# Kernel tuning notes

Measured on AMD Instinct MI355X. Metric: run time of the kernel, lower is better.

The kernel has to match this reference:

```python
import jax, jax.numpy as jnp
import numpy as np
from jax import lax

B, T, N, D = 64, 2048, 64, 128


def setup_inputs() -> dict:
    key = jax.random.key(0)
    k0, k1, k2, k3, k4 = jax.random.split(key, 5)
    return {
        "X": jax.random.normal(k0, (B, T, D), dtype=jnp.float32),
        "transition_matrix": jax.random.uniform(k1, (N, N), dtype=jnp.float32) / N,
        "state_priors": jax.random.uniform(k2, (N,), dtype=jnp.float32) / N,
        "means": jax.random.normal(k3, (N, D), dtype=jnp.float32),
        "log_vars": jax.random.normal(k4, (N, D), dtype=jnp.float32) * 0.1,
    }


def _emission_logprobs(X, means, log_vars):
    # Diagonal-Gaussian log density per state, vectorized over (B,T,N).
    # sum_d (x-mu)^2 / var expanded into GEMMs to avoid a (B,T,N,D) tensor.
    inv_var = jnp.exp(-log_vars)                               # (N,D)
    t1 = jnp.einsum('btd,nd->btn', X * X, inv_var)             # sum x^2/var
    t2 = jnp.einsum('btd,nd->btn', X, means * inv_var)         # sum x*mu/var
    t3 = jnp.sum(means * means * inv_var + log_vars, axis=-1)  # (N,)
    d = X.shape[-1]
    log2pi = jnp.log(jnp.asarray(2.0 * np.pi, dtype=X.dtype))
    return -0.5 * (t1 - 2.0 * t2 + t3 + d * log2pi)            # (B,T,N)


def reference(X, transition_matrix, state_priors, means, log_vars):
    log_A = jax.nn.log_softmax(transition_matrix, axis=1)      # (N,N)
    log_pi = jax.nn.log_softmax(state_priors, axis=0)          # (N,)
    log_b = _emission_logprobs(X, means, log_vars)             # (B,T,N)

    alpha0 = log_pi + log_b[:, 0]                              # (B,N)
    lb_rest = jnp.moveaxis(log_b[:, 1:], 1, 0)                 # (T-1,B,N)

    def step(alpha_prev, lb_t):
        # alpha_t[j] = log_b_t[j] + logsumexp_i(alpha_{t-1}[i] + log_A[i,j])
        scores = alpha_prev[:, :, None] + log_A[None, :, :]    # (B,N,N)
        alpha_t = lb_t + jax.scipy.special.logsumexp(scores, axis=1)
        return alpha_t, None

    alpha_T, _ = lax.scan(step, alpha0, lb_rest)
    # original gathers log-sum at the last timestep, then sums over subjects
    return jnp.sum(jax.scipy.special.logsumexp(alpha_T, axis=-1))
```

## Files before the change

kernel.cpp:

```cpp
#include <hip/hip_runtime.h>


constexpr int ATF_OFF  = 0;
constexpr int PI_OFF   = 2048;
constexpr int CN_OFF   = 2112;
constexpr int WBF_OFF  = 2176;
constexpr int MV_OFF   = 10368;
constexpr int PART_OFF = 141440;
constexpr int GLS_OFF  = 141504;
constexpr int E0G_OFF  = 145600;
constexpr int G_OFF    = 149696;

typedef __attribute__((ext_vector_type(8))) short bf16x8;
typedef __attribute__((ext_vector_type(16))) float f32x16;

union BU { unsigned u[4]; bf16x8 v; };

__device__ inline float wave_max(float v) {
  #pragma unroll
  for (int off = 1; off < 64; off <<= 1) v = fmaxf(v, __shfl_xor(v, off));
  return v;
}
__device__ inline float wave_sum(float v) {
  #pragma unroll
  for (int off = 1; off < 64; off <<= 1) v += __shfl_xor(v, off);
  return v;
}
__device__ inline float read_lane(float v, int l) {
  return __uint_as_float(__builtin_amdgcn_readlane(__float_as_uint(v), l));
}
__device__ inline unsigned f2bf(float f) {
  unsigned u = __float_as_uint(f);
  u += 0x7FFFu + ((u >> 16) & 1u);
  return u >> 16;
}
__device__ inline unsigned cvt_pk(float lo, float hi) {
  unsigned r;
  asm("v_cvt_pk_bf16_f32 %0, %1, %2" : "=v"(r) : "v"(lo), "v"(hi));
  return r;
}

__global__ void setup_kernel(const float* __restrict__ trans,
                             const float* __restrict__ priors,
                             const float* __restrict__ means,
                             const float* __restrict__ log_vars,
                             float* __restrict__ ws) {
  __shared__ float Psh[64 * 64];
  int tid = threadIdx.x, blk = blockIdx.x;

  if (blk == 0) {
    int lane = tid & 63, w = tid >> 6;
    for (int r = 0; r < 16; ++r) {
      int i = w * 16 + r;
      float x = trans[i * 64 + lane];
      float m = wave_max(x);
      float s = wave_sum(__expf(x - m));
      Psh[i * 64 + lane] = __expf(x - (m + __logf(s)));
    }
    if (w == 0) {
      float x = priors[lane];
      float m = wave_max(x);
      float s = wave_sum(__expf(x - m));
      ws[PI_OFF + lane] = __expf(x - (m + __logf(s)));
    }
    __syncthreads();
    for (int idx = tid; idx < 512; idx += 256) {
      int f = idx >> 6, l = idx & 63;
      int I = f >> 2, Kb = f & 3;
      int m = 32 * I + (l & 31);
      int kb = 16 * Kb + 8 * (l >> 5);
      unsigned u[4];
      #pragma unroll
      for (int p = 0; p < 4; ++p) {
        unsigned a = f2bf(Psh[(kb + 2 * p) * 64 + m]);
        unsigned b = f2bf(Psh[(kb + 2 * p + 1) * 64 + m]);
        u[p] = a | (b << 16);
      }
      *reinterpret_cast<uint4*>(&ws[ATF_OFF + idx * 4]) = make_uint4(u[0], u[1], u[2], u[3]);
    }
  } else if (blk <= 8) {
    int idx = (blk - 1) * 256 + tid;
    int f = idx >> 6, l = idx & 63;
    int Kb = f >> 1, J = f & 1;
    int n = 32 * J + (l & 31);
    int kb = 16 * Kb + 8 * (l >> 5);
    unsigned u[4];
    #pragma unroll
    for (int p = 0; p < 4; ++p) {
      int k0 = kb + 2 * p, k1 = k0 + 1;
      int d0 = k0 & 127, d1 = k1 & 127;
      float iv0 = __expf(-log_vars[n * 128 + d0]);
      float iv1 = __expf(-log_vars[n * 128 + d1]);
      float a  = (k0 < 128) ? (-0.5f * iv0) : (means[n * 128 + d0] * iv0);
      float bb = (k1 < 128) ? (-0.5f * iv1) : (means[n * 128 + d1] * iv1);
      u[p] = f2bf(a) | (f2bf(bb) << 16);
    }
    *reinterpret_cast<uint4*>(&ws[WBF_OFF + idx * 4]) = make_uint4(u[0], u[1], u[2], u[3]);
  } else {
    float* part = Psh;
    int n = tid & 63, g = tid >> 6;
    float s = 0.f;
    for (int d = 32 * g; d < 32 * g + 32; ++d) {
      float lv = log_vars[n * 128 + d];
      float mu = means[n * 128 + d];
      s += mu * mu * __expf(-lv) + lv;
    }
    part[g * 64 + n] = s;
    __syncthreads();
    if (tid < 64) {
      float tot = (part[tid] + part[64 + tid]) + (part[128 + tid] + part[192 + tid]);
      ws[CN_OFF + tid] = -0.5f * (tot + 128.0f * 1.8378770664093453f);
    }
  }
}

__global__ __launch_bounds__(128, 4) void fused_scan(const float* __restrict__ X,
                                                     float* __restrict__ ws) {
  __shared__ __align__(16) unsigned short Esh[64 * 64];

  const int tid = threadIdx.x;
  const int lane = tid & 63, J = tid >> 6;
  const int h = lane >> 5, il = lane & 31;
  const int job = blockIdx.x, b = job >> 5, cch = job & 31;
  const int tstart = 1 + cch * 64;
  const int len = (cch == 31) ? 63 : 64;

  {
    int i_lane = J * 32 + il;
    int t_lane = tstart + i_lane;
    if (cch == 31 && i_lane == 63) t_lane = 0;
    const float* Xr = X + ((size_t)b * 2048 + t_lane) * 128;

    bf16x8 ax[8], asq[8];
    #pragma unroll
    for (int s = 0; s < 8; ++s) {
      float4 v0 = *reinterpret_cast<const float4*>(Xr + s * 16 + 8 * h);
      float4 v1 = *reinterpret_cast<const float4*>(Xr + s * 16 + 8 * h + 4);
      BU bx, bq;
      bx.u[0] = cvt_pk(v0.x, v0.y); bx.u[1] = cvt_pk(v0.z, v0.w);
      bx.u[2] = cvt_pk(v1.x, v1.y); bx.u[3] = cvt_pk(v1.z, v1.w);
      bq.u[0] = cvt_pk(v0.x * v0.x, v0.y * v0.y);
      bq.u[1] = cvt_pk(v0.z * v0.z, v0.w * v0.w);
      bq.u[2] = cvt_pk(v1.x * v1.x, v1.y * v1.y);
      bq.u[3] = cvt_pk(v1.z * v1.z, v1.w * v1.w);
      ax[s] = bx.v; asq[s] = bq.v;
    }

    const uint4* wbf = reinterpret_cast<const uint4*>(&ws[WBF_OFF]);
    f32x16 acc0, acc1;
    #pragma unroll
    for (int z = 0; z < 16; ++z) { acc0[z] = 0.f; acc1[z] = 0.f; }
    #pragma unroll
    for (int Kb = 0; Kb < 8; ++Kb) {
      BU b0, b1;
      *reinterpret_cast<uint4*>(b0.u) = wbf[(2 * Kb + 0) * 64 + lane];
      *reinterpret_cast<uint4*>(b1.u) = wbf[(2 * Kb + 1) * 64 + lane];
      acc0 = __builtin_amdgcn_mfma_f32_32x32x16_bf16(asq[Kb], b0.v, acc0, 0, 0, 0);
      acc1 = __builtin_amdgcn_mfma_f32_32x32x16_bf16(asq[Kb], b1.v, acc1, 0, 0, 0);
    }
    #pragma unroll
    for (int Kb = 8; Kb < 16; ++Kb) {
      BU b0, b1;
      *reinterpret_cast<uint4*>(b0.u) = wbf[(2 * Kb + 0) * 64 + lane];
      *reinterpret_cast<uint4*>(b1.u) = wbf[(2 * Kb + 1) * 64 + lane];
      acc0 = __builtin_amdgcn_mfma_f32_32x32x16_bf16(ax[Kb - 8], b0.v, acc0, 0, 0, 0);
      acc1 = __builtin_amdgcn_mfma_f32_32x32x16_bf16(ax[Kb - 8], b1.v, acc1, 0, 0, 0);
    }

    float cn0 = ws[CN_OFF + il];
    float cn1 = ws[CN_OFF + 32 + il];
    float* MVp = &ws[MV_OFF] + (size_t)b * 2048;
    #pragma unroll
    for (int e = 0; e < 16; ++e) {
      float v0 = acc0[e] + cn0;
      float v1 = acc1[e] + cn1;
      float mx = fmaxf(v0, v1);
      #pragma unroll
      for (int off = 1; off < 32; off <<= 1) mx = fmaxf(mx, __shfl_xor(mx, off));
      int r = 32 * J + (e & 3) + 8 * (e >> 2) + 4 * h;
      float e0 = __expf(v0 - mx), e1 = __expf(v1 - mx);
      if (cch == 31 && r == 63) {
        ws[E0G_OFF + b * 64 + il]      = e0;
        ws[E0G_OFF + b * 64 + 32 + il] = e1;
        if (il == 0) MVp[0] = mx;
      } else {
        Esh[r * 64 + il]      = (unsigned short)f2bf(e0);
        Esh[r * 64 + 32 + il] = (unsigned short)f2bf(e1);
        if (il == 0) MVp[tstart + r] = mx;
      }
    }
  }
  __syncthreads();

  bf16x8 atf0, atf1, atf2, atf3, atf4, atf5, atf6, atf7;
  atf0 = *reinterpret_cast<const bf16x8*>(&ws[ATF_OFF + (0 * 64 + lane) * 4]);
  atf1 = *reinterpret_cast<const bf16x8*>(&ws[ATF_OFF + (1 * 64 + lane) * 4]);
  atf2 = *reinterpret_cast<const bf16x8*>(&ws[ATF_OFF + (2 * 64 + lane) * 4]);
  atf3 = *reinterpret_cast<const bf16x8*>(&ws[ATF_OFF + (3 * 64 + lane) * 4]);
  atf4 = *reinterpret_cast<const bf16x8*>(&ws[ATF_OFF + (4 * 64 + lane) * 4]);
  atf5 = *reinterpret_cast<const bf16x8*>(&ws[ATF_OFF + (5 * 64 + lane) * 4]);
  atf6 = *reinterpret_cast<const bf16x8*>(&ws[ATF_OFF + (6 * 64 + lane) * 4]);
  atf7 = *reinterpret_cast<const bf16x8*>(&ws[ATF_OFF + (7 * 64 + lane) * 4]);

  bf16x8 bf0, bf1, bf2, bf3;
  {
    int js0 = 32 * J + il - 8 * h;
#define IDF(dst, Kb) { int js = js0 - 16 * (Kb); BU bu_;                      \
    _Pragma("unroll")                                                         \
    for (int p = 0; p < 4; ++p)                                               \
      bu_.u[p] = ((js >> 1) == p) ? ((js & 1) ? 0x3F800000u : 0x00003F80u) : 0u; \
    dst = bu_.v; }
    IDF(bf0, 0) IDF(bf1, 1) IDF(bf2, 2) IDF(bf3, 3)
#undef IDF
  }

  float Ls = 0.0f;

#define LOADE(dst, idx) {                                                     \
    const char* Ep_ = reinterpret_cast<const char*>(Esh) + (size_t)(idx) * 128; \
    _Pragma("unroll")                                                         \
    for (int q_ = 0; q_ < 4; ++q_) {                                          \
      dst[q_]     = *reinterpret_cast<const uint2*>(Ep_ + 16 * q_ + 8 * h);   \
      dst[4 + q_] = *reinterpret_cast<const uint2*>(Ep_ + 64 + 16 * q_ + 8 * h); \
    } }

#define SX(W, z, I)                                                           \
  ({ uint2 u_ = W[4 * (I) + ((z) >> 2)];                                      \
     unsigned w_ = (((z) >> 1) & 1) ? u_.y : u_.x;                            \
     __uint_as_float(((z) & 1) ? (w_ & 0xFFFF0000u) : (w_ << 16)); })

#define BBS(dst, At, p, I, W) {                                               \
    unsigned xe0 = cvt_pk((At)[8*(p)+0] * SX(W, 8*(p)+0, I),                  \
                          (At)[8*(p)+1] * SX(W, 8*(p)+1, I));                 \
    unsigned xe1 = cvt_pk((At)[8*(p)+2] * SX(W, 8*(p)+2, I),                  \
                          (At)[8*(p)+3] * SX(W, 8*(p)+3, I));                 \
    unsigned xo0 = cvt_pk((At)[8*(p)+4] * SX(W, 8*(p)+4, I),                  \
                          (At)[8*(p)+5] * SX(W, 8*(p)+5, I));                 \
    unsigned xo1 = cvt_pk((At)[8*(p)+6] * SX(W, 8*(p)+6, I),                  \
                          (At)[8*(p)+7] * SX(W, 8*(p)+7, I));                 \
    asm("v_permlane32_swap_b32 %0, %1" : "+v"(xe0), "+v"(xo0));               \
    asm("v_permlane32_swap_b32 %0, %1" : "+v"(xe1), "+v"(xo1));               \
    BU bu_; bu_.u[0] = xe0; bu_.u[1] = xe1; bu_.u[2] = xo0; bu_.u[3] = xo1;   \
    dst = bu_.v; }

#define MFMA_HEAD(d, A, B)                                                    \
    asm("v_mfma_f32_32x32x16_bf16 %0, %1, %2, 0"                              \
        : "=&v"(d) : "v"(A), "v"(B));
#define MFMA_ACC(d, A, B)                                                     \
    asm("v_mfma_f32_32x32x16_bf16 %0, %1, %2, %0"                             \
        : "+v"(d) : "v"(A), "v"(B));

#define STEP(EW, DO_RN) {                                                     \
    f32x16 a0, a1;                                                            \
    MFMA_HEAD(a0, atf0, bf0)                                                  \
    MFMA_HEAD(a1, atf4, bf0)                                                  \
    MFMA_ACC(a0, atf1, bf1)                                                   \
    MFMA_ACC(a1, atf5, bf1)                                                   \
    MFMA_ACC(a0, atf2, bf2)                                                   \
    MFMA_ACC(a1, atf6, bf2)                                                   \
    MFMA_ACC(a0, atf3, bf3)                                                   \
    MFMA_ACC(a1, atf7, bf3)                                                   \
    asm volatile("s_nop 7\n\ts_nop 7\n\ts_nop 3" : "+v"(a0), "+v"(a1));       \
    if (DO_RN) {                                                              \
      float mx = 0.f;                                                         \
      _Pragma("unroll")                                                       \
      for (int z = 0; z < 16; ++z) mx = fmaxf(mx, fmaxf(a0[z], a1[z]));       \
      mx = wave_max(mx);                                                      \
      float inv = 1.0f / mx;                                                  \
      Ls += __logf(mx);                                                       \
      _Pragma("unroll")                                                       \
      for (int z = 0; z < 16; ++z) { a0[z] *= inv; a1[z] *= inv; }            \
    }                                                                         \
    BBS(bf0, a0, 0, 0, EW) BBS(bf1, a0, 1, 0, EW)                             \
    BBS(bf2, a1, 0, 1, EW) BBS(bf3, a1, 1, 1, EW) }

  uint2 eA[8];
  #pragma unroll 1
  for (int step = 0; step < len; ++step) {
    LOADE(eA, step);
    STEP(eA, ((step & 7) == 7));
  }

#undef STEP
#undef MFMA_ACC
#undef MFMA_HEAD
#undef BBS
#undef SX
#undef LOADE

  unsigned short* Gb = reinterpret_cast<unsigned short*>(&ws[G_OFF]) + (size_t)job * 4096;
#define GST(fr, Kb) { BU bu_; bu_.v = fr;                                     \
    _Pragma("unroll")                                                         \
    for (int p = 0; p < 4; ++p) {                                             \
      int k = 16 * (Kb) + 8 * h + 2 * p;                                      \
      Gb[k * 64 + 32 * J + il]       = (unsigned short)(bu_.u[p] & 0xFFFFu);  \
      Gb[(k + 1) * 64 + 32 * J + il] = (unsigned short)(bu_.u[p] >> 16);      \
    } }
  GST(bf0, 0) GST(bf1, 1) GST(bf2, 2) GST(bf3, 3)
#undef GST
  if (lane == 0) ws[GLS_OFF + job * 2 + J] = Ls;
}

__global__ __launch_bounds__(64, 1) void fwd2_combine(float* __restrict__ ws) {
  int b = blockIdx.x, j = threadIdx.x;

  float Ms = 0.f;
  for (int k = 0; k < 32; ++k) Ms += ws[MV_OFF + (size_t)b * 2048 + k * 64 + j];
  Ms = wave_sum(Ms);

  float w = ws[PI_OFF + j] * ws[E0G_OFF + b * 64 + j];
  float Lacc = Ms;

  const unsigned short* Gb =
      reinterpret_cast<const unsigned short*>(&ws[G_OFF]) + (size_t)b * 32 * 4096;
  const uint4* gbase = reinterpret_cast<const uint4*>(Gb);

  uint4 gw[8];
  #pragma unroll
  for (int s = 0; s < 8; ++s) gw[s] = gbase[j * 4 + s];

  for (int c = 0; c < 32; ++c) {
    uint4 gn[8];
    int cnx = (c + 1 < 32) ? (c + 1) : c;
    #pragma unroll
    for (int s = 0; s < 8; ++s) gn[s] = gbase[(size_t)cnx * 256 + j * 4 + s];

    float gv[64];
    #pragma unroll
    for (int s = 0; s < 8; ++s) {
      gv[8 * s + 0] = __uint_as_float(gw[s].x << 16);
      gv[8 * s + 1] = __uint_as_float(gw[s].x & 0xFFFF0000u);
      gv[8 * s + 2] = __uint_as_float(gw[s].y << 16);
      gv[8 * s + 3] = __uint_as_float(gw[s].y & 0xFFFF0000u);
      gv[8 * s + 4] = __uint_as_float(gw[s].z << 16);
      gv[8 * s + 5] = __uint_as_float(gw[s].z & 0xFFFF0000u);
      gv[8 * s + 6] = __uint_as_float(gw[s].w << 16);
      gv[8 * s + 7] = __uint_as_float(gw[s].w & 0xFFFF0000u);
    }
    float l0 = 0.f, l1 = 0.f, h0 = 0.f, h1 = 0.f;
    #pragma unroll
    for (int i = 0; i < 32; i += 2) {
      l0 = fmaf(read_lane(w, i + 0), gv[i + 0], l0);
      l1 = fmaf(read_lane(w, i + 1), gv[i + 1], l1);
      h0 = fmaf(read_lane(w, 32 + i + 0), gv[32 + i + 0], h0);
      h1 = fmaf(read_lane(w, 32 + i + 1), gv[32 + i + 1], h1);
    }
    float ylo = l0 + l1, yhi = h0 + h1;
    float g0 = ws[GLS_OFF + (b * 32 + c) * 2 + 0];
    float g1 = ws[GLS_OFF + (b * 32 + c) * 2 + 1];
    float Lm = fmaxf(g0, g1);
    float y = __expf(g0 - Lm) * ylo + __expf(g1 - Lm) * yhi;
    float s = wave_sum(y);
    w = y * (1.0f / s);
    Lacc += Lm + __logf(s);

    #pragma unroll
    for (int s2 = 0; s2 < 8; ++s2) gw[s2] = gn[s2];
  }
  float S = wave_sum(w);
  if (j == 0) ws[PART_OFF + b] = Lacc + __logf(S);
}

__global__ void final_kernel(const float* __restrict__ part, float* __restrict__ out) {
  float v = part[threadIdx.x];
  float s = wave_sum(v);
  if (threadIdx.x == 0) out[0] = s;
}

extern "C" void kernel_launch(void* const* d_in, const int* in_sizes, int n_in,
                              void* d_out, int out_size, void* d_ws, size_t ws_size,
                              hipStream_t stream) {
  const float* X        = (const float*)d_in[0];
  const float* trans    = (const float*)d_in[1];
  const float* priors   = (const float*)d_in[2];
  const float* means    = (const float*)d_in[3];
  const float* log_vars = (const float*)d_in[4];
  float* ws  = (float*)d_ws;
  float* out = (float*)d_out;

  hipLaunchKernelGGL(setup_kernel, dim3(10), dim3(256), 0, stream,
                     trans, priors, means, log_vars, ws);
  hipLaunchKernelGGL(fused_scan, dim3(2048), dim3(128), 0, stream, X, ws);
  hipLaunchKernelGGL(fwd2_combine, dim3(64), dim3(64), 0, stream, ws);
  hipLaunchKernelGGL(final_kernel, dim3(1), dim3(64), 0, stream,
                     ws + PART_OFF, out);
}
```

Baseline: 124.9 us.

## Halve time-chunk length to 32 and split emission MFMA across waves

Doubles the number of time chunks per sequence from 32 to 64, so each fused_scan block handles 32 timesteps and 4096 blocks are launched. The emission GEMM is now split so each wave computes one 32-state half, with a shared-memory row-max exchange, and launch bounds are raised to allow more resident blocks. This aims for more parallelism and a shorter per-block serial chain. In exchange it doubles the serial chunk-combine loop in fwd2_combine and the G matrix traffic. The hidden part of the scan code that depends on chunk length is not shown updated, so correctness there is uncertain.

```diff
diff --git a/kernel.cpp b/kernel.cpp
--- a/kernel.cpp
+++ b/kernel.cpp
@@ -8,8 +8,8 @@
 constexpr int MV_OFF   = 10368;
 constexpr int PART_OFF = 141440;
 constexpr int GLS_OFF  = 141504;
-constexpr int E0G_OFF  = 145600;
-constexpr int G_OFF    = 149696;
+constexpr int E0G_OFF  = 149696;
+constexpr int G_OFF    = 153792;
 
 typedef __attribute__((ext_vector_type(8))) short bf16x8;
 typedef __attribute__((ext_vector_type(16))) float f32x16;
@@ -114,21 +114,21 @@
   }
 }
 
-__global__ __launch_bounds__(128, 4) void fused_scan(const float* __restrict__ X,
+__global__ __launch_bounds__(128, 6) void fused_scan(const float* __restrict__ X,
                                                      float* __restrict__ ws) {
-  __shared__ __align__(16) unsigned short Esh[64 * 64];
+  __shared__ __align__(16) unsigned short Esh[32 * 64];
+  __shared__ float Mrow[2][32];
 
   const int tid = threadIdx.x;
   const int lane = tid & 63, J = tid >> 6;
   const int h = lane >> 5, il = lane & 31;
-  const int job = blockIdx.x, b = job >> 5, cch = job & 31;
-  const int tstart = 1 + cch * 64;
-  const int len = (cch == 31) ? 63 : 64;
+  const int job = blockIdx.x, b = job >> 6, cch = job & 63;
+  const int tstart = 1 + cch * 32;
+  const int len = (cch == 63) ? 31 : 32;
 
   {
-    int i_lane = J * 32 + il;
-    int t_lane = tstart + i_lane;
-    if (cch == 31 && i_lane == 63) t_lane = 0;
+    int t_lane = tstart + il;
+    if (cch == 63 && il == 31) t_lane = 0;
     const float* Xr = X + ((size_t)b * 2048 + t_lane) * 128;
 
     bf16x8 ax[8], asq[8];
@@ -147,46 +147,46 @@
     }
 
     const uint4* wbf = reinterpret_cast<const uint4*>(&ws[WBF_OFF]);
-    f32x16 acc0, acc1;
-    #pragma unroll
-    for (int z = 0; z < 16; ++z) { acc0[z] = 0.f; acc1[z] = 0.f; }
+    f32x16 acc;
+    #pragma unroll
+    for (int z = 0; z < 16; ++z) acc[z] = 0.f;
     #pragma unroll
     for (int Kb = 0; Kb < 8; ++Kb) {
-      BU b0, b1;
-      *reinterpret_cast<uint4*>(b0.u) = wbf[(2 * Kb + 0) * 64 + lane];
-      *reinterpret_cast<uint4*>(b1.u) = wbf[(2 * Kb + 1) * 64 + lane];
-      acc0 = __builtin_amdgcn_mfma_f32_32x32x16_bf16(asq[Kb], b0.v, acc0, 0, 0, 0);
-      acc1 = __builtin_amdgcn_mfma_f32_32x32x16_bf16(asq[Kb], b1.v, acc1, 0, 0, 0);
+      BU bb;
+      *reinterpret_cast<uint4*>(bb.u) = wbf[(2 * Kb + J) * 64 + lane];
+      acc = __builtin_amdgcn_mfma_f32_32x32x16_bf16(asq[Kb], bb.v, acc, 0, 0, 0);
     }
     #pragma unroll
     for (int Kb = 8; Kb < 16; ++Kb) {
-      BU b0, b1;
-      *reinterpret_cast<uint4*>(b0.u) = wbf[(2 * Kb + 0) * 64 + lane];
-      *reinterpret_cast<uint4*>(b1.u) = wbf[(2 * Kb + 1) * 64 + lane];
-      acc0 = __builtin_amdgcn_mfma_f32_32x32x16_bf16(ax[Kb - 8], b0.v, acc0, 0, 0, 0);
-      acc1 = __builtin_amdgcn_mfma_f32_32x32x16_bf16(ax[Kb - 8], b1.v, acc1, 0, 0, 0);
-    }
-
-    float cn0 = ws[CN_OFF + il];
-    float cn1 = ws[CN_OFF + 32 + il];
+      BU bb;
+      *reinterpret_cast<uint4*>(bb.u) = wbf[(2 * Kb + J) * 64 + lane];
+      acc = __builtin_amdgcn_mfma_f32_32x32x16_bf16(ax[Kb - 8], bb.v, acc, 0, 0, 0);
+    }
+
+    float cnv = ws[CN_OFF + 32 * J + il];
+    #pragma unroll
+    for (int e = 0; e < 16; ++e) {
+      float v = acc[e] + cnv;
+      float pm = v;
+      #pragma unroll
+      for (int off = 1; off < 32; off <<= 1) pm = fmaxf(pm, __shfl_xor(pm, off));
+      int r = (e & 3) + 8 * (e >> 2) + 4 * h;
+      if (il == 0) Mrow[J][r] = pm;
+    }
+    __syncthreads();
     float* MVp = &ws[MV_OFF] + (size_t)b * 2048;
     #pragma unroll
     for (int e = 0; e < 16; ++e) {
-      float v0 = acc0[e] + cn0;
-      float v1 = acc1[e] + cn1;
-      float mx = fmaxf(v0, v1);
-      #pragma unroll
-      for (int off = 1; off < 32; off <<= 1) mx = fmaxf(mx, __shfl_xor(mx, off));
-      int r = 32 * J + (e & 3) + 8 * (e >> 2) + 4 * h;
-      float e0 = __expf(v0 - mx), e1 = __expf(v1 - mx);
-      if (cch == 31 && r == 63) {
-        ws[E0G_OFF + b * 64 + il]      = e0;
-        ws[E0G_OFF + b * 64 + 32 + il] = e1;
-        if (il == 0) MVp[0] = mx;
+      float v = acc[e] + cnv;
+      int r = (e & 3) + 8 * (e >> 2) + 4 * h;
+      float mx = fmaxf(Mrow[0][r], Mrow[1][r]);
+      float ev = __expf(v - mx);
+      if (cch == 63 && r == 31) {
+        ws[E0G_OFF + b * 64 + 32 * J + il] = ev;
+        if (il == 0 && J == 0) MVp[0] = mx;
       } else {
-        Esh[r * 64 + il]      = (unsigned short)f2bf(e0);
-        Esh[r * 64 + 32 + il] = (unsigned short)f2bf(e1);
-        if (il == 0) MVp[tstart + r] = mx;
+        Esh[r * 64 + 32 * J + il] = (unsigned short)f2bf(ev);
+        if (il == 0 && J == 0) MVp[tstart + r] = mx;
       }
     }
   }
@@ -312,16 +312,16 @@
   float Lacc = Ms;
 
   const unsigned short* Gb =
-      reinterpret_cast<const unsigned short*>(&ws[G_OFF]) + (size_t)b * 32 * 4096;
+      reinterpret_cast<const unsigned short*>(&ws[G_OFF]) + (size_t)b * 64 * 4096;
   const uint4* gbase = reinterpret_cast<const uint4*>(Gb);
 
   uint4 gw[8];
   #pragma unroll
   for (int s = 0; s < 8; ++s) gw[s] = gbase[j * 4 + s];
 
-  for (int c = 0; c < 32; ++c) {
+  for (int c = 0; c < 64; ++c) {
     uint4 gn[8];
-    int cnx = (c + 1 < 32) ? (c + 1) : c;
+    int cnx = (c + 1 < 64) ? (c + 1) : c;
     #pragma unroll
     for (int s = 0; s < 8; ++s) gn[s] = gbase[(size_t)cnx * 256 + j * 4 + s];
 
@@ -346,8 +346,8 @@
       h1 = fmaf(read_lane(w, 32 + i + 1), gv[32 + i + 1], h1);
     }
     float ylo = l0 + l1, yhi = h0 + h1;
-    float g0 = ws[GLS_OFF + (b * 32 + c) * 2 + 0];
-    float g1 = ws[GLS_OFF + (b * 32 + c) * 2 + 1];
+    float g0 = ws[GLS_OFF + (b * 64 + c) * 2 + 0];
+    float g1 = ws[GLS_OFF + (b * 64 + c) * 2 + 1];
     float Lm = fmaxf(g0, g1);
     float y = __expf(g0 - Lm) * ylo + __expf(g1 - Lm) * yhi;
     float s = wave_sum(y);
@@ -380,7 +380,7 @@
 
   hipLaunchKernelGGL(setup_kernel, dim3(10), dim3(256), 0, stream,
                      trans, priors, means, log_vars, ws);
-  hipLaunchKernelGGL(fused_scan, dim3(2048), dim3(128), 0, stream, X, ws);
+  hipLaunchKernelGGL(fused_scan, dim3(4096), dim3(128), 0, stream, X, ws);
   hipLaunchKernelGGL(fwd2_combine, dim3(64), dim3(64), 0, stream, ws);
   hipLaunchKernelGGL(final_kernel, dim3(1), dim3(64), 0, stream,
                      ws + PART_OFF, out);
```

After: 175.2 us. 40.4% more time.
